# Optimization experiments

Measured on AMD Instinct MI355X. Metric: run time of the kernel, lower is better.

The kernel has to match this reference:

```python
import jax, jax.numpy as jnp
import numpy as np

NUM_HEADS = 8
NUM_POINTS = 4


def setup_inputs() -> dict:
    key = jax.random.key(0)
    ks = jax.random.split(key, 8)
    B, N, C, H, W = 8, 8192, 256, 128, 128
    HP2 = NUM_HEADS * NUM_POINTS * 2
    HP = NUM_HEADS * NUM_POINTS
    query = jax.random.normal(ks[0], (B, N, C), jnp.float32)
    reference_points = jax.random.uniform(ks[1], (B, N, 2), dtype=jnp.float32)
    value = jax.random.normal(ks[2], (B, C, H, W), jnp.float32)
    # learned params (offset gen is zero-init in the original; use small random
    W_off = jax.random.normal(ks[3], (C, HP2), jnp.float32) * 0.02
    b_off = jnp.zeros((HP2,), jnp.float32)
    W_attn = jax.random.normal(ks[4], (C, HP), jnp.float32) * (1.0 / np.sqrt(C))
    b_attn = jnp.zeros((HP,), jnp.float32)
    W_out = jax.random.normal(ks[5], (C, C), jnp.float32) * (1.0 / np.sqrt(C))
    b_out = jnp.zeros((C,), jnp.float32)
    return dict(query=query, reference_points=reference_points, value=value,
                W_off=W_off, b_off=b_off, W_attn=W_attn, b_attn=b_attn,
                W_out=W_out, b_out=b_out, H=H, W=W)


def reference(query, reference_points, value, W_off, b_off, W_attn, b_attn,
              W_out, b_out, H, W):
    B, N, C = query.shape
    Hh, P = NUM_HEADS, NUM_POINTS
    D = C // Hh

    offset = (query @ W_off + b_off).reshape(B, N, Hh, P, 2)
    attn = jax.nn.softmax((query @ W_attn + b_attn).reshape(B, N, Hh, P), axis=-1)

    # sampling locations in grid_sample convention: (x, y) in [-1, 1]
    ref = reference_points * 2.0 - 1.0
    loc = ref[:, :, None, None, :] + offset  # (B, N, Hh, P, 2)

    # value -> (B, Hh, H*W, D)
    val = value.reshape(B, Hh, D, H, W).transpose(0, 1, 3, 4, 2).reshape(B, Hh, H * W, D)

    # align_corners=False pixel coordinates
    x = (loc[..., 0] + 1.0) * (W * 0.5) - 0.5  # (B, N, Hh, P)
    y = (loc[..., 1] + 1.0) * (H * 0.5) - 0.5
    x0f = jnp.floor(x); y0f = jnp.floor(y)
    wx1 = x - x0f; wy1 = y - y0f
    x0 = x0f.astype(jnp.int32); y0 = y0f.astype(jnp.int32)
    x1 = x0 + 1; y1 = y0 + 1

    def gather(ix, iy, w):
        # bilinear corner gather with zero padding (mask out-of-bounds)
        valid = (ix >= 0) & (ix < W) & (iy >= 0) & (iy < H)
        idx = jnp.clip(iy, 0, H - 1) * W + jnp.clip(ix, 0, W - 1)  # (B,N,Hh,P)
        idx_t = idx.transpose(0, 2, 1, 3).reshape(B, Hh, N * P)
        g = jnp.take_along_axis(val, idx_t[..., None], axis=2)  # (B,Hh,N*P,D)
        g = g.reshape(B, Hh, N, P, D).transpose(0, 2, 1, 3, 4)  # (B,N,Hh,P,D)
        return g * (w * valid)[..., None]

    sampled = (gather(x0, y0, (1 - wx1) * (1 - wy1))
               + gather(x1, y0, wx1 * (1 - wy1))
               + gather(x0, y1, (1 - wx1) * wy1)
               + gather(x1, y1, wx1 * wy1))  # (B,N,Hh,P,D)

    out = jnp.einsum('bnhk,bnhkd->bnhd', attn, sampled).reshape(B, N, C)
    return out @ W_out + b_out
```

## Files before the change

### kernel.cpp

```cpp
#include <hip/hip_runtime.h>
#include <hip/hip_bf16.h>
#include <hip/hip_fp16.h>
#include <cstddef>

#define B_  8
#define N_  8192
#define C_  256
#define H_  128
#define W_  128
#define HH  8
#define PP  4
#define DD  32
#define HW  (H_ * W_)

typedef short bf16x8 __attribute__((ext_vector_type(8)));
typedef _Float16 f16x8 __attribute__((ext_vector_type(8)));
typedef float f32x4  __attribute__((ext_vector_type(4)));

static __device__ __forceinline__ short f2bf_s(float f) {
    __hip_bfloat16 b = __float2bfloat16(f);
    return *reinterpret_cast<short*>(&b);
}
static __device__ __forceinline__ float bf_s2f(short s) {
    __hip_bfloat16 b = *reinterpret_cast<__hip_bfloat16*>(&s);
    return __bfloat162float(b);
}

__global__ __launch_bounds__(256) void kTP(const float* __restrict__ value,
                                           __half* __restrict__ val,
                                           const float* __restrict__ W_off,
                                           const float* __restrict__ W_attn,
                                           short* __restrict__ Wc_hi,
                                           short* __restrict__ Wc_lo,
                                           const float* __restrict__ Wsrc,
                                           __half* __restrict__ Wt) {
    __shared__ __align__(16) char smem[33024];
    const int t   = threadIdx.x;
    const int bid = blockIdx.x;

    if (bid < 4096) {
        float (*tile)[257] = (float (*)[257])smem;
        const int bh   = bid >> 6;
        const int pix0 = (bid & 63) * 256;
        const float* src = value + (size_t)bh * 32 * HW + pix0;
#pragma unroll
        for (int i = 0; i < 8; ++i) {
            int d  = i * 4 + (t >> 6);
            int p4 = t & 63;
            float4 v = *(const float4*)&src[(size_t)d * HW + p4 * 4];
            tile[d][p4 * 4 + 0] = v.x;
            tile[d][p4 * 4 + 1] = v.y;
            tile[d][p4 * 4 + 2] = v.z;
            tile[d][p4 * 4 + 3] = v.w;
        }
        __syncthreads();
#pragma unroll
        for (int j = 0; j < 4; ++j) {
            int pix = j * 64 + (t >> 2);
            int d0  = (t & 3) * 8;
            short o[8];
#pragma unroll
            for (int k = 0; k < 8; ++k) {
                __half hh = __float2half(tile[d0 + k][pix]);
                o[k] = *reinterpret_cast<short*>(&hh);
            }
            *(bf16x8*)&val[((size_t)bh * HW + pix0 + pix) * 32 + d0] =
                *(bf16x8*)o;
        }
    } else if (bid < 4192) {
        const int c = bid - 4096;
        float v = (c < 64) ? W_off[(size_t)t * 64 + c]
                           : W_attn[(size_t)t * 32 + (c - 64)];
        short h = f2bf_s(v);
        short l = f2bf_s(v - bf_s2f(h));
        Wc_hi[(size_t)c * 256 + t] = h;
        Wc_lo[(size_t)c * 256 + t] = l;
    } else {
        float (*tile)[65] = (float (*)[65])smem;
        const int bx = bid - 4192;
        const int n0 = (bx & 3) * 64;
        const int k0 = (bx >> 2) * 64;
#pragma unroll
        for (int i = 0; i < 16; ++i) {
            int kk = i * 4 + (t >> 6);
            int nn = t & 63;
            tile[kk][nn] = Wsrc[(size_t)(k0 + kk) * 256 + n0 + nn];
        }
        __syncthreads();
#pragma unroll
        for (int i = 0; i < 16; ++i) {
            int nn = i * 4 + (t >> 6);
            int kk = t & 63;
            Wt[(size_t)(n0 + nn) * 256 + k0 + kk] = __float2half(tile[kk][nn]);
        }
    }
}

__global__ __launch_bounds__(256) void kA1M(const float* __restrict__ query,
                                            const float* __restrict__ refp,
                                            const short* __restrict__ Wc_hi,
                                            const short* __restrict__ Wc_lo,
                                            const float* __restrict__ b_off,
                                            const float* __restrict__ b_attn,
                                            float4* __restrict__ locattn) {
    __shared__ __align__(16) char smem[57344];
    short* As_hi = (short*)smem;
    short* As_lo = (short*)(smem + 16384);
    short* Bs_hi = (short*)(smem + 32768);
    short* Bs_lo = (short*)(smem + 45056);
    float* Ct    = (float*)smem;

    const int t    = threadIdx.x;
    const int lane = t & 63;
    const int w    = t >> 6;
    const int wm   = (w & 1) * 64;
    const int wn   = (w >> 1) * 48;
    const int quad = lane >> 4;
    const int l16  = lane & 15;
    const int row0 = blockIdx.x * 128;

    f32x4 acc[4][3];
#pragma unroll
    for (int mt = 0; mt < 4; ++mt)
#pragma unroll
        for (int nt = 0; nt < 3; ++nt)
            acc[mt][nt] = (f32x4){0.f, 0.f, 0.f, 0.f};

    for (int k0c = 0; k0c < 4; ++k0c) {
#pragma unroll
        for (int i = 0; i < 8; ++i) {
            int f   = t + i * 256;
            int row = f >> 4;
            int kq4 = f & 15;
            float4 q = *(const float4*)&query[(size_t)(row0 + row) * 256 +
                                              k0c * 64 + kq4 * 4];
            short4 hv, lv;
            hv.x = f2bf_s(q.x); lv.x = f2bf_s(q.x - bf_s2f(hv.x));
            hv.y = f2bf_s(q.y); lv.y = f2bf_s(q.y - bf_s2f(hv.y));
            hv.z = f2bf_s(q.z); lv.z = f2bf_s(q.z - bf_s2f(hv.z));
            hv.w = f2bf_s(q.w); lv.w = f2bf_s(q.w - bf_s2f(hv.w));
            int base = row * 64 + (((kq4 >> 1) ^ (row & 7)) * 8) + (kq4 & 1) * 4;
            *(short4*)&As_hi[base] = hv;
            *(short4*)&As_lo[base] = lv;
        }
#pragma unroll
        for (int i = 0; i < 3; ++i) {
            int idx = t + i * 256;
            int n   = idx >> 3;
            int kb  = idx & 7;
            int dst = n * 64 + ((kb ^ (n & 7)) * 8);
            *(uint4*)&Bs_hi[dst] =
                *(const uint4*)&Wc_hi[(size_t)n * 256 + k0c * 64 + kb * 8];
            *(uint4*)&Bs_lo[dst] =
                *(const uint4*)&Wc_lo[(size_t)n * 256 + k0c * 64 + kb * 8];
        }
        __syncthreads();

#pragma unroll
        for (int ks = 0; ks < 2; ++ks) {
            const int kq = ks * 4 + quad;
            bf16x8 ah[4], al[4], bh[3], bl[3];
#pragma unroll
            for (int mt = 0; mt < 4; ++mt) {
                int m = wm + mt * 16 + l16;
                ah[mt] = *(const bf16x8*)&As_hi[m * 64 + (kq ^ (m & 7)) * 8];
                al[mt] = *(const bf16x8*)&As_lo[m * 64 + (kq ^ (m & 7)) * 8];
            }
#pragma unroll
            for (int nt = 0; nt < 3; ++nt) {
                int n = wn + nt * 16 + l16;
                bh[nt] = *(const bf16x8*)&Bs_hi[n * 64 + (kq ^ (n & 7)) * 8];
                bl[nt] = *(const bf16x8*)&Bs_lo[n * 64 + (kq ^ (n & 7)) * 8];
            }
#pragma unroll
            for (int mt = 0; mt < 4; ++mt)
#pragma unroll
                for (int nt = 0; nt < 3; ++nt)
                    acc[mt][nt] = __builtin_amdgcn_mfma_f32_16x16x32_bf16(
                        ah[mt], bh[nt], acc[mt][nt], 0, 0, 0);
#pragma unroll
            for (int mt = 0; mt < 4; ++mt)
#pragma unroll
                for (int nt = 0; nt < 3; ++nt)
                    acc[mt][nt] = __builtin_amdgcn_mfma_f32_16x16x32_bf16(
                        ah[mt], bl[nt], acc[mt][nt], 0, 0, 0);
#pragma unroll
            for (int mt = 0; mt < 4; ++mt)
#pragma unroll
                for (int nt = 0; nt < 3; ++nt)
                    acc[mt][nt] = __builtin_amdgcn_mfma_f32_16x16x32_bf16(
                        al[mt], bh[nt], acc[mt][nt], 0, 0, 0);
        }
        __syncthreads();
    }

#pragma unroll
    for (int mt = 0; mt < 4; ++mt) {
#pragma unroll
        for (int nt = 0; nt < 3; ++nt) {
            int col = wn + nt * 16 + l16;
#pragma unroll
            for (int rI = 0; rI < 4; ++rI) {
                int row = wm + mt * 16 + quad * 4 + rI;
                Ct[row * 100 + col] = acc[mt][nt][rI];
            }
        }
    }
    __syncthreads();

    const int rg = t >> 3;
    const int h  = t & 7;
    float boff[8];
#pragma unroll
    for (int j = 0; j < 8; ++j) boff[j] = b_off[h * 8 + j];
    float batn[4];
#pragma unroll
    for (int j = 0; j < 4; ++j) batn[j] = b_attn[h * 4 + j];

#pragma unroll
    for (int r = 0; r < 4; ++r) {
        int row  = rg * 4 + r;
        int rowg = row0 + row;
        float rx = refp[(size_t)rowg * 2 + 0];
        float ry = refp[(size_t)rowg * 2 + 1];
        float4 lg4 = *(const float4*)&Ct[row * 100 + 64 + h * 4];
        float lg[4] = {lg4.x + batn[0], lg4.y + batn[1],
                       lg4.z + batn[2], lg4.w + batn[3]};
        float m = fmaxf(fmaxf(lg[0], lg[1]), fmaxf(lg[2], lg[3]));
        float e[4];
        float s = 0.f;
#pragma unroll
        for (int p = 0; p < 4; ++p) { e[p] = __expf(lg[p] - m); s += e[p]; }
        float inv = 1.f / s;
        float4 o0 = *(const float4*)&Ct[row * 100 + h * 8];
        float4 o1 = *(const float4*)&Ct[row * 100 + h * 8 + 4];
        float ox[4] = {o0.x + boff[0], o0.z + boff[2],
                       o1.x + boff[4], o1.z + boff[6]};
        float oy[4] = {o0.y + boff[1], o0.w + boff[3],
                       o1.y + boff[5], o1.w + boff[7]};
#pragma unroll
        for (int p = 0; p < 4; ++p) {
            float x = (rx * 2.f + ox[p]) * (W_ * 0.5f) - 0.5f;
            float y = (ry * 2.f + oy[p]) * (H_ * 0.5f) - 0.5f;
            locattn[(size_t)rowg * 32 + h * 4 + p] =
                make_float4(x, y, e[p] * inv, 0.f);
        }
    }
}

__global__ __launch_bounds__(256) void kAC(const float4* __restrict__ locattn,
                                           const __half* __restrict__ val,
                                           const __half* __restrict__ Wt,
                                           const float* __restrict__ bias,
                                           float* __restrict__ out) {
    __shared__ __align__(16) char smem[65536];
    char*  midc = smem;
    uint4* ow   = (uint4*)(smem + 32768);
    short* Bs   = (short*)(smem + 32768);

    const int t    = threadIdx.x;
    const int bid  = blockIdx.x;
    const int b    = bid & 7;
    const int n0   = (bid >> 3) * 64;

    const int pn  = t >> 3;
    const int pkb = t & 7;
    uint4 pre[8];
#pragma unroll
    for (int i = 0; i < 8; ++i) {
        int n = pn + i * 32;
        pre[i] = *(const uint4*)&Wt[(size_t)n * 256 + pkb * 8];
    }

#pragma unroll
    for (int i = 0; i < 8; ++i) {
        int item = t + i * 256;
        int r  = item >> 5;
        int hp = item & 31;
        float4 L = locattn[((size_t)b * N_ + n0 + r) * 32 + hp];
        float x = L.x, y = L.y, a = L.z;
        float xf = floorf(x), yf = floorf(y);
        int x0 = (int)xf, y0 = (int)yf;
        int x1 = x0 + 1, y1 = y0 + 1;
        float wx1 = x - xf, wy1 = y - yf;
        float wx0 = 1.f - wx1, wy0 = 1.f - wy1;
        int cx0 = min(max(x0, 0), W_ - 1);
        int cx1 = min(max(x1, 0), W_ - 1);
        int cy0 = min(max(y0, 0), H_ - 1);
        int cy1 = min(max(y1, 0), H_ - 1);
        bool bx0 = (x0 >= 0) & (x0 < W_);
        bool bx1 = (x1 >= 0) & (x1 < W_);
        bool by0 = (y0 >= 0) & (y0 < H_);
        bool by1 = (y1 >= 0) & (y1 < H_);
        float f00 = a * wx0 * wy0 * ((bx0 & by0) ? 1.f : 0.f);
        float f10 = a * wx1 * wy0 * ((bx1 & by0) ? 1.f : 0.f);
        float f01 = a * wx0 * wy1 * ((bx0 & by1) ? 1.f : 0.f);
        float f11 = a * wx1 * wy1 * ((bx1 & by1) ? 1.f : 0.f);
        uint4 rec;
        rec.x = (unsigned)(cy0 * W_ + cx0) | ((unsigned)(cy0 * W_ + cx1) << 16);
        rec.y = (unsigned)(cy1 * W_ + cx0) | ((unsigned)(cy1 * W_ + cx1) << 16);
        __half2 wA = __floats2half2_rn(f00, f10);
        __half2 wB = __floats2half2_rn(f01, f11);
        rec.z = *reinterpret_cast<unsigned*>(&wA);
        rec.w = *reinterpret_cast<unsigned*>(&wB);
        ow[item] = rec;
    }
    __syncthreads();

    {
        const int j8 = t & 7;
        const int g  = t >> 3;
        const int d8 = j8 * 4;
#pragma unroll
        for (int q = 0; q < 16; ++q) {
            int pair = g * 16 + q;
            int r = pair >> 3;
            int h = pair & 7;
            const char* vb = (const char*)val +
                ((((size_t)b * 8 + h) * HW) * 32 + d8) * 2;
            __half2 a01 = __float2half2_rn(0.f);
            __half2 a23 = __float2half2_rn(0.f);
#pragma unroll
            for (int p = 0; p < 4; ++p) {
                uint4 rec = ow[r * 32 + h * 4 + p];
                int i0 = rec.x & 0xffff, i1 = rec.x >> 16;
                int i2 = rec.y & 0xffff, i3 = rec.y >> 16;
                __half2 wA = *reinterpret_cast<__half2*>(&rec.z);
                __half2 wB = *reinterpret_cast<__half2*>(&rec.w);
                uint2 u0 = *(const uint2*)(vb + (size_t)i0 * 64);
                uint2 u1 = *(const uint2*)(vb + (size_t)i1 * 64);
                uint2 u2 = *(const uint2*)(vb + (size_t)i2 * 64);
                uint2 u3 = *(const uint2*)(vb + (size_t)i3 * 64);
                __half2 w00 = __low2half2(wA);
                a01 = __hfma2(*reinterpret_cast<__half2*>(&u0.x), w00, a01);
                a23 = __hfma2(*reinterpret_cast<__half2*>(&u0.y), w00, a23);
                __half2 w10 = __high2half2(wA);
                a01 = __hfma2(*reinterpret_cast<__half2*>(&u1.x), w10, a01);
                a23 = __hfma2(*reinterpret_cast<__half2*>(&u1.y), w10, a23);
                __half2 w01 = __low2half2(wB);
                a01 = __hfma2(*reinterpret_cast<__half2*>(&u2.x), w01, a01);
                a23 = __hfma2(*reinterpret_cast<__half2*>(&u2.y), w01, a23);
                __half2 w11 = __high2half2(wB);
                a01 = __hfma2(*reinterpret_cast<__half2*>(&u3.x), w11, a01);
                a23 = __hfma2(*reinterpret_cast<__half2*>(&u3.y), w11, a23);
            }
            int c8  = h * 4 + (d8 >> 3);
            int off = r * 512 + ((c8 ^ (r & 7)) * 16) + (d8 & 7) * 2;
            uint2 st;
            st.x = *reinterpret_cast<unsigned*>(&a01);
            st.y = *reinterpret_cast<unsigned*>(&a23);
            *(uint2*)(midc + off) = st;
        }
    }
    __syncthreads();

    const int lane = t & 63;
    const int w    = t >> 6;
    const int wn   = w * 64;
    const int quad = lane >> 4;
    const int l16  = lane & 15;

    f32x4 acc[4][4];
#pragma unroll
    for (int mt = 0; mt < 4; ++mt)
#pragma unroll
        for (int nt = 0; nt < 4; ++nt)
            acc[mt][nt] = (f32x4){0.f, 0.f, 0.f, 0.f};

    for (int k0 = 0; k0 < 4; ++k0) {
#pragma unroll
        for (int i = 0; i < 8; ++i) {
            int n = pn + i * 32;
            *(uint4*)&Bs[n * 64 + ((pkb ^ (n & 7)) * 8)] = pre[i];
        }
        if (k0 < 3) {
#pragma unroll
            for (int i = 0; i < 8; ++i) {
                int n = pn + i * 32;
                pre[i] = *(const uint4*)&Wt[(size_t)n * 256 +
                                            (k0 + 1) * 64 + pkb * 8];
            }
        }
        __syncthreads();

#pragma unroll
        for (int ks = 0; ks < 2; ++ks) {
            const int kq = ks * 4 + quad;
            f16x8 af[4], bfv[4];
#pragma unroll
            for (int mt = 0; mt < 4; ++mt) {
                int m = mt * 16 + l16;
                af[mt] = *(const f16x8*)(midc + m * 512 +
                                         (((k0 * 8 + kq) ^ (m & 7)) * 16));
            }
#pragma unroll
            for (int nt = 0; nt < 4; ++nt) {
                int n = wn + nt * 16 + l16;
                bfv[nt] = *(const f16x8*)&Bs[n * 64 + ((kq ^ (n & 7)) * 8)];
            }
#pragma unroll
            for (int mt = 0; mt < 4; ++mt)
#pragma unroll
                for (int nt = 0; nt < 4; ++nt)
                    acc[mt][nt] = __builtin_amdgcn_mfma_f32_16x16x32_f16(
                        af[mt], bfv[nt], acc[mt][nt], 0, 0, 0);
        }
        __syncthreads();
    }

#pragma unroll
    for (int nt = 0; nt < 4; ++nt) {
        int col  = wn + nt * 16 + l16;
        float bv = bias[col];
#pragma unroll
        for (int mt = 0; mt < 4; ++mt) {
#pragma unroll
            for (int rI = 0; rI < 4; ++rI) {
                int r = mt * 16 + quad * 4 + rI;
                out[((size_t)b * N_ + n0 + r) * 256 + col] =
                    acc[mt][nt][rI] + bv;
            }
        }
    }
}

extern "C" void kernel_launch(void* const* d_in, const int* in_sizes, int n_in,
                              void* d_out, int out_size, void* d_ws, size_t ws_size,
                              hipStream_t stream) {
    const float* query  = (const float*)d_in[0];
    const float* refp   = (const float*)d_in[1];
    const float* value  = (const float*)d_in[2];
    const float* W_off  = (const float*)d_in[3];
    const float* b_off  = (const float*)d_in[4];
    const float* W_attn = (const float*)d_in[5];
    const float* b_attn = (const float*)d_in[6];
    const float* W_out  = (const float*)d_in[7];
    const float* b_out  = (const float*)d_in[8];
    float* out = (float*)d_out;

    char*   ws      = (char*)d_ws;
    __half* val     = (__half*)(ws);
    float4* locattn = (float4*)(ws + 67108864);
    __half* Wt      = (__half*)(ws + 134217728);
    short*  Wc_hi   = (short*)(ws + 134348800);
    short*  Wc_lo   = (short*)(ws + 134397952);

    kTP <<<dim3(4208), 256, 0, stream>>>(value, val, W_off, W_attn,
                                         Wc_hi, Wc_lo, W_out, Wt);
    kA1M<<<dim3((B_ * N_) / 128), 256, 0, stream>>>(query, refp, Wc_hi, Wc_lo,
                                                    b_off, b_attn, locattn);
    kAC <<<dim3((B_ * N_) / 64), 256, 0, stream>>>(locattn, val, Wt,
                                                   b_out, out);
}
```

Before: 405.5 us.

## Halve kAC row tile to raise occupancy and stage coalesced output through LDS

```diff
diff --git a/kernel.cpp b/kernel.cpp
--- a/kernel.cpp
+++ b/kernel.cpp
@@ -248,32 +248,23 @@
     }
 }
 
-__global__ __launch_bounds__(256) void kAC(const float4* __restrict__ locattn,
-                                           const __half* __restrict__ val,
-                                           const __half* __restrict__ Wt,
-                                           const float* __restrict__ bias,
-                                           float* __restrict__ out) {
-    __shared__ __align__(16) char smem[65536];
+__global__ __launch_bounds__(256, 4) void kAC(const float4* __restrict__ locattn,
+                                              const __half* __restrict__ val,
+                                              const __half* __restrict__ Wt,
+                                              const float* __restrict__ bias,
+                                              float* __restrict__ out) {
+    __shared__ __align__(16) char smem[32768];
     char*  midc = smem;
-    uint4* ow   = (uint4*)(smem + 32768);
-    short* Bs   = (short*)(smem + 32768);
-
-    const int t    = threadIdx.x;
-    const int bid  = blockIdx.x;
-    const int b    = bid & 7;
-    const int n0   = (bid >> 3) * 64;
-
-    const int pn  = t >> 3;
-    const int pkb = t & 7;
-    uint4 pre[8];
-#pragma unroll
-    for (int i = 0; i < 8; ++i) {
-        int n = pn + i * 32;
-        pre[i] = *(const uint4*)&Wt[(size_t)n * 256 + pkb * 8];
-    }
-
-#pragma unroll
-    for (int i = 0; i < 8; ++i) {
+    uint4* ow   = (uint4*)(smem + 16384);
+    short* Bs   = (short*)(smem + 16384);
+
+    const int t   = threadIdx.x;
+    const int bid = blockIdx.x;
+    const int b   = bid & 7;
+    const int n0  = (bid >> 3) * 32;
+
+#pragma unroll
+    for (int i = 0; i < 4; ++i) {
         int item = t + i * 256;
         int r  = item >> 5;
         int hp = item & 31;
@@ -303,7 +294,7 @@
         __half2 wB = __floats2half2_rn(f01, f11);
         rec.z = *reinterpret_cast<unsigned*>(&wA);
         rec.w = *reinterpret_cast<unsigned*>(&wB);
-        ow[item] = rec;
+        ow[r * 32 + (hp ^ (r & 7))] = rec;
     }
     __syncthreads();
 
@@ -312,17 +303,14 @@
         const int g  = t >> 3;
         const int d8 = j8 * 4;
 #pragma unroll
-        for (int q = 0; q < 16; ++q) {
-            int pair = g * 16 + q;
-            int r = pair >> 3;
-            int h = pair & 7;
+        for (int q = 0; q < 8; ++q) {
             const char* vb = (const char*)val +
-                ((((size_t)b * 8 + h) * HW) * 32 + d8) * 2;
+                (((size_t)b * 8 + q) * HW * 32 + d8) * 2;
             __half2 a01 = __float2half2_rn(0.f);
             __half2 a23 = __float2half2_rn(0.f);
 #pragma unroll
             for (int p = 0; p < 4; ++p) {
-                uint4 rec = ow[r * 32 + h * 4 + p];
+                uint4 rec = ow[g * 32 + ((q * 4 + p) ^ (g & 7))];
                 int i0 = rec.x & 0xffff, i1 = rec.x >> 16;
                 int i2 = rec.y & 0xffff, i3 = rec.y >> 16;
                 __half2 wA = *reinterpret_cast<__half2*>(&rec.z);
@@ -344,8 +332,8 @@
                 a01 = __hfma2(*reinterpret_cast<__half2*>(&u3.x), w11, a01);
                 a23 = __hfma2(*reinterpret_cast<__half2*>(&u3.y), w11, a23);
             }
-            int c8  = h * 4 + (d8 >> 3);
-            int off = r * 512 + ((c8 ^ (r & 7)) * 16) + (d8 & 7) * 2;
+            int c8  = q * 4 + (j8 >> 1);
+            int off = g * 512 + ((c8 ^ (g & 7)) * 16) + (j8 & 1) * 8;
             uint2 st;
             st.x = *reinterpret_cast<unsigned*>(&a01);
             st.y = *reinterpret_cast<unsigned*>(&a23);
@@ -360,67 +348,69 @@
     const int quad = lane >> 4;
     const int l16  = lane & 15;
 
-    f32x4 acc[4][4];
-#pragma unroll
-    for (int mt = 0; mt < 4; ++mt)
+    f32x4 acc[2][4];
+#pragma unroll
+    for (int mt = 0; mt < 2; ++mt)
 #pragma unroll
         for (int nt = 0; nt < 4; ++nt)
             acc[mt][nt] = (f32x4){0.f, 0.f, 0.f, 0.f};
 
-    for (int k0 = 0; k0 < 4; ++k0) {
-#pragma unroll
-        for (int i = 0; i < 8; ++i) {
-            int n = pn + i * 32;
-            *(uint4*)&Bs[n * 64 + ((pkb ^ (n & 7)) * 8)] = pre[i];
-        }
-        if (k0 < 3) {
-#pragma unroll
-            for (int i = 0; i < 8; ++i) {
-                int n = pn + i * 32;
-                pre[i] = *(const uint4*)&Wt[(size_t)n * 256 +
-                                            (k0 + 1) * 64 + pkb * 8];
-            }
-        }
-        __syncthreads();
-
-#pragma unroll
-        for (int ks = 0; ks < 2; ++ks) {
-            const int kq = ks * 4 + quad;
-            f16x8 af[4], bfv[4];
-#pragma unroll
-            for (int mt = 0; mt < 4; ++mt) {
-                int m = mt * 16 + l16;
-                af[mt] = *(const f16x8*)(midc + m * 512 +
-                                         (((k0 * 8 + kq) ^ (m & 7)) * 16));
-            }
-#pragma unroll
-            for (int nt = 0; nt < 4; ++nt) {
-                int n = wn + nt * 16 + l16;
-                bfv[nt] = *(const f16x8*)&Bs[n * 64 + ((kq ^ (n & 7)) * 8)];
-            }
-#pragma unroll
-            for (int mt = 0; mt < 4; ++mt)
-#pragma unroll
-                for (int nt = 0; nt < 4; ++nt)
-                    acc[mt][nt] = __builtin_amdgcn_mfma_f32_16x16x32_f16(
-                        af[mt], bfv[nt], acc[mt][nt], 0, 0, 0);
-        }
-        __syncthreads();
-    }
-
+    for (int k0 = 0; k0 < 8; ++k0) {
+#pragma unroll
+        for (int i = 0; i < 4; ++i) {
+            int idx = t + i * 256;
+            int n   = idx >> 2;
+            int kb  = idx & 3;
+            *(uint4*)&Bs[n * 32 + ((kb ^ (n & 3)) * 8)] =
+                *(const uint4*)&Wt[(size_t)n * 256 + k0 * 32 + kb * 8];
+        }
+        __syncthreads();
+
+        f16x8 af[2], bfv[4];
+#pragma unroll
+        for (int mt = 0; mt < 2; ++mt) {
+            int m = mt * 16 + l16;
+            af[mt] = *(const f16x8*)(midc + m * 512 +
+                                     (((k0 * 4 + quad) ^ (m & 7)) * 16));
+        }
+#pragma unroll
+        for (int nt = 0; nt < 4; ++nt) {
+            int n = wn + nt * 16 + l16;
+            bfv[nt] = *(const f16x8*)&Bs[n * 32 + ((quad ^ (n & 3)) * 8)];
+        }
+#pragma unroll
+        for (int mt = 0; mt < 2; ++mt)
+#pragma unroll
+            for (int nt = 0; nt < 4; ++nt)
+                acc[mt][nt] = __builtin_amdgcn_mfma_f32_16x16x32_f16(
+                    af[mt], bfv[nt], acc[mt][nt], 0, 0, 0);
+        __syncthreads();
+    }
+
+    float* ost = (float*)smem;
 #pragma unroll
     for (int nt = 0; nt < 4; ++nt) {
         int col  = wn + nt * 16 + l16;
         float bv = bias[col];
 #pragma unroll
-        for (int mt = 0; mt < 4; ++mt) {
+        for (int mt = 0; mt < 2; ++mt) {
 #pragma unroll
             for (int rI = 0; rI < 4; ++rI) {
-                int r = mt * 16 + quad * 4 + rI;
-                out[((size_t)b * N_ + n0 + r) * 256 + col] =
-                    acc[mt][nt][rI] + bv;
-            }
-        }
+                int row = mt * 16 + quad * 4 + rI;
+                int byt = row * 1024 + ((col * 4) ^ ((row & 1) << 6));
+                *(float*)((char*)ost + byt) = acc[mt][nt][rI] + bv;
+            }
+        }
+    }
+    __syncthreads();
+#pragma unroll
+    for (int i = 0; i < 8; ++i) {
+        int idx = t + i * 256;
+        int row = idx >> 6;
+        int u   = idx & 63;
+        float4 v = *(const float4*)((char*)ost +
+                                    row * 1024 + ((u * 16) ^ ((row & 1) << 6)));
+        *(float4*)&out[((size_t)b * N_ + n0 + row) * 256 + u * 4] = v;
     }
 }
 
@@ -449,6 +439,6 @@
                                          Wc_hi, Wc_lo, W_out, Wt);
     kA1M<<<dim3((B_ * N_) / 128), 256, 0, stream>>>(query, refp, Wc_hi, Wc_lo,
                                                     b_off, b_attn, locattn);
-    kAC <<<dim3((B_ * N_) / 64), 256, 0, stream>>>(locattn, val, Wt,
+    kAC <<<dim3((B_ * N_) / 32), 256, 0, stream>>>(locattn, val, Wt,
                                                    b_out, out);
 }
```

After: 362.7 us. -10.6%, faster.
